# Kernel optimization log

Measured on AMD Instinct MI355X. Metric: run time of the kernel, lower is better.

## Reference

```python
import jax, jax.numpy as jnp
import numpy as np

EMBED_DIM = 1024
ATTEN_DIM = 64


def setup_inputs() -> dict:
    key = jax.random.key(0)
    k_x, k_q, k_k, k_v = jax.random.split(key, 4)
    B, S = 4, 4096
    scale = 1.0 / np.sqrt(EMBED_DIM)
    x = jax.random.normal(k_x, (B, S, EMBED_DIM), dtype=jnp.float32)
    # torch nn.Linear weights are [out_features, in_features]
    Wq = jax.random.normal(k_q, (ATTEN_DIM, EMBED_DIM), dtype=jnp.float32) * scale
    Wk = jax.random.normal(k_k, (ATTEN_DIM, EMBED_DIM), dtype=jnp.float32) * scale
    Wv = jax.random.normal(k_v, (ATTEN_DIM, EMBED_DIM), dtype=jnp.float32) * scale
    return {"x": x, "Wq": Wq, "Wk": Wk, "Wv": Wv}


def reference(x, Wq, Wk, Wv):
    # q, k, v: [B, S, D]
    q = jnp.einsum('bse,de->bsd', x, Wq)
    k = jnp.einsum('bse,de->bsd', x, Wk)
    v = jnp.einsum('bse,de->bsd', x, Wv)
    d = k.shape[-1]
    scores = jnp.einsum('bsd,btd->bst', q, k) / jnp.sqrt(jnp.float32(d))
    S = x.shape[1]
    causal = jnp.tril(jnp.ones((S, S), dtype=bool))
    scores = jnp.where(causal[None, :, :], scores, -jnp.inf)
    attn = jax.nn.softmax(scores, axis=-1)
    return jnp.einsum('bst,btd->bsd', attn, v)
```

## Files before the change

### kernel.cpp

```cpp
#include <hip/hip_runtime.h>
#include <hip/hip_bf16.h>
#include <stdint.h>

typedef __attribute__((ext_vector_type(8))) short  short8;
typedef __attribute__((ext_vector_type(4))) short  short4v;
typedef __attribute__((ext_vector_type(4))) float  float4v;

#define MFMA16(a, b, c) __builtin_amdgcn_mfma_f32_16x16x32_bf16((a), (b), (c), 0, 0, 0)

#define S_LEN  4096
#define NBATCH 4
#define EMB    1024
#define DD     64
#define NROWS  (NBATCH * S_LEN)
#define SCL2   0.1803368801111204f

#define AS1 const __attribute__((address_space(1))) unsigned int*
#define AS3 __attribute__((address_space(3))) unsigned int*

static __device__ __forceinline__ short f2bf(float f) {
  uint32_t u = __float_as_uint(f);
  return (short)((u + 0x7FFFu + ((u >> 16) & 1u)) >> 16);
}
static __device__ __forceinline__ unsigned pk2(float a, float b) {
  union { __hip_bfloat162 h; unsigned u; } z;
  z.h = __float22bfloat162_rn(make_float2(a, b));
  return z.u;
}
static __device__ __forceinline__ short8 cvt8(float4v a, float4v b) {
  union { unsigned u[4]; short8 s; } z;
  z.u[0] = pk2(a[0], a[1]); z.u[1] = pk2(a[2], a[3]);
  z.u[2] = pk2(b[0], b[1]); z.u[3] = pk2(b[2], b[3]);
  return z.s;
}

__global__ void wcvt_kernel(const float* __restrict__ Wq, const float* __restrict__ Wk,
                            const float* __restrict__ Wv, short* __restrict__ Wb2) {
  const int t   = blockIdx.x * 256 + threadIdx.x;
  const int row = t >> 7;
  const int k   = (t & 127) * 8;
  const float* src = (row < 64) ? (Wq + (size_t)row * EMB)
                   : (row < 128) ? (Wk + (size_t)(row - 64) * EMB)
                                 : (Wv + (size_t)(row - 128) * EMB);
  const float sc = (row < 64) ? SCL2 : 1.0f;
  float4v a = *(const float4v*)(src + k);
  float4v b = *(const float4v*)(src + k + 4);
#pragma unroll
  for (int i = 0; i < 4; ++i) { a[i] *= sc; b[i] *= sc; }
  *(short8*)(Wb2 + (((k >> 5) * 192 + row) << 5) + (k & 31)) = cvt8(a, b);
}

__global__ __launch_bounds__(256, 2) void qkv_kernel(
    const float* __restrict__ x, const short* __restrict__ Wb2,
    short* __restrict__ Qb, short* __restrict__ Kb, short* __restrict__ Vt) {
  __shared__ float As[2][2048];
  __shared__ short Bs[2][12288];

  const int tid  = threadIdx.x;
  const int w    = tid >> 6;
  const int lane = tid & 63;
  const int ln   = lane & 15;
  const int quad = lane >> 4;
  const int m0   = blockIdx.x * 32;
  const int wr   = w & 1;
  const int wc   = w >> 1;

  const int tA0 = 2 * w, tA1 = 2 * w + 1;
  const float* xA0 = x + (size_t)(m0 + ((tA0 >> 2) << 4) + (lane >> 2)) * EMB
                       + ((tA0 & 3) * 4 + (lane & 3)) * 4;
  const float* xA1 = x + (size_t)(m0 + ((tA1 >> 2) << 4) + (lane >> 2)) * EMB
                       + ((tA1 & 3) * 4 + (lane & 3)) * 4;
  const short* wB = Wb2 + (size_t)(6 * w) * 512 + lane * 8;

#define STAGE(S, BUF) do {                                                      \
    __builtin_amdgcn_global_load_lds((AS1)(xA0 + (S) * 64),                     \
        (AS3)&As[BUF][tA0 * 256], 16, 0, 0);                                    \
    __builtin_amdgcn_global_load_lds((AS1)(xA1 + (S) * 64),                     \
        (AS3)&As[BUF][tA1 * 256], 16, 0, 0);                                    \
    _Pragma("unroll")                                                           \
    for (int j = 0; j < 6; ++j)                                                 \
      __builtin_amdgcn_global_load_lds((AS1)(wB + (size_t)(S) * 12288 + j * 512),\
          (AS3)&Bs[BUF][(6 * w + j) * 512], 16, 0, 0);                          \
  } while (0)

  const float4v zz = {0.f, 0.f, 0.f, 0.f};
  float4v acc[6] = {zz, zz, zz, zz, zz, zz};

  STAGE(0, 0);
  int buf = 0;
  for (int s = 0; s < 16; ++s) {
    __syncthreads();
    if (s + 1 < 16) STAGE(s + 1, buf ^ 1);
    short8 aF[2];
#pragma unroll
    for (int h = 0; h < 2; ++h) {
      const int ai = (wr * 4 + 2 * h + (quad >> 1)) * 256 + (ln * 4 + (quad & 1) * 2) * 4;
      const float4v lo = *(const float4v*)&As[buf][ai];
      const float4v hi = *(const float4v*)&As[buf][ai + 4];
      aF[h] = cvt8(lo, hi);
    }
#pragma unroll
    for (int f = 0; f < 6; ++f) {
      const int cf = wc * 6 + f;
      const short8 b0 = *(const short8*)&Bs[buf][(cf * 16 + ln) * 32 + quad * 8];
      const short8 b1 = *(const short8*)&Bs[buf][6144 + (cf * 16 + ln) * 32 + quad * 8];
      if (wc == 0 || f < 2) {
        acc[f] = MFMA16(aF[0], b0, acc[f]);
        acc[f] = MFMA16(aF[1], b1, acc[f]);
      } else {
        acc[f] = MFMA16(b0, aF[0], acc[f]);
        acc[f] = MFMA16(b1, aF[1], acc[f]);
      }
    }
    buf ^= 1;
  }
#undef STAGE

  const int b  = m0 >> 12;
  const int sb = m0 & (S_LEN - 1);
  if (wc == 0) {
#pragma unroll
    for (int f = 0; f < 6; ++f)
#pragma unroll
      for (int r = 0; r < 4; ++r) {
        const int row = m0 + wr * 16 + quad * 4 + r;
        if (f < 4) Qb[(size_t)row * DD + f * 16 + ln] = f2bf(acc[f][r]);
        else       Kb[(size_t)row * DD + (f - 4) * 16 + ln] = f2bf(acc[f][r]);
      }
  } else {
#pragma unroll
    for (int f = 0; f < 2; ++f)
#pragma unroll
      for (int r = 0; r < 4; ++r) {
        const int row = m0 + wr * 16 + quad * 4 + r;
        Kb[(size_t)row * DD + 32 + f * 16 + ln] = f2bf(acc[f][r]);
      }
#pragma unroll
    for (int f = 2; f < 6; ++f)
#pragma unroll
      for (int r = 0; r < 4; ++r) {
        const int d = (f - 2) * 16 + quad * 4 + r;
        Vt[((size_t)b * DD + d) * S_LEN + sb + wr * 16 + ln] = f2bf(acc[f][r]);
      }
  }
}

__global__ __launch_bounds__(256, 2) void attn_kernel(
    const short* __restrict__ Qb, const short* __restrict__ Kb,
    const short* __restrict__ Vt, float* __restrict__ out) {
  __shared__ short kvbuf[4][2][4096];
  __shared__ float pbuf[4][16 * 36];
  __shared__ float llds[4][16];

  const int tid  = threadIdx.x;
  const int w    = tid >> 6;
  const int lane = tid & 63;
  const int ln   = lane & 15;
  const int quad = lane >> 4;
  const int g    = blockIdx.x;
  const int b    = g & 3;
  const int j    = g >> 2;

  const short* Kbase = Kb + (size_t)b * S_LEN * DD;
  const short* Vbase = Vt + (size_t)b * DD * S_LEN;
  const int koff = (lane & 7) * DD + (lane >> 3) * 8;
  const size_t voff = (size_t)(lane & 15) * S_LEN + (lane >> 4) * 8;
  float* pw = &pbuf[w][0];
  const float4v zz = {0.f, 0.f, 0.f, 0.f};

#define KVSTAGE(KV0, BUF) do {                                                  \
    const short* kp_ = Kbase + (size_t)(KV0) * DD + koff;                       \
    const short* vp_ = Vbase + (KV0) + voff;                                    \
    _Pragma("unroll")                                                           \
    for (int s5 = 0; s5 < 4; ++s5)                                              \
      __builtin_amdgcn_global_load_lds((AS1)(kp_ + s5 * 8 * DD),                \
          (AS3)&kvbuf[w][BUF][s5 * 512], 16, 0, 0);                             \
    _Pragma("unroll")                                                           \
    for (int s5 = 0; s5 < 4; ++s5)                                              \
      __builtin_amdgcn_global_load_lds((AS1)(vp_ + (size_t)(s5 * 16) * S_LEN),  \
          (AS3)&kvbuf[w][BUF][2048 + s5 * 512], 16, 0, 0);                      \
  } while (0)

  for (int ph = 0; ph < 2; ++ph) {
    const int band = ph ? (255 - j) : j;
    const int qb   = band * 16;
    const int qg0  = b * S_LEN + qb;
    const int T    = (qb + 47) >> 5;

    short8 aQ[2];
#pragma unroll
    for (int h = 0; h < 2; ++h)
      aQ[h] = *(const short8*)(Qb + (size_t)(qg0 + ln) * DD + h * 32 + quad * 8);

    float4v o[4] = {zz, zz, zz, zz};
    float lp[4]  = {0.f, 0.f, 0.f, 0.f};

    if (w < T) KVSTAGE(w * 32, 0);
    int buf = 0;

    for (int it = w; it < T; it += 4) {
      const int kv0 = it * 32;
      asm volatile("s_waitcnt vmcnt(0)" ::: "memory");
      const short* kb_ = &kvbuf[w][buf][0];
      const short* vb_ = &kvbuf[w][buf][2048];

      short8 kf[2][2];
#pragma unroll
      for (int ct = 0; ct < 2; ++ct)
#pragma unroll
        for (int h = 0; h < 2; ++h)
          kf[ct][h] = *(const short8*)(kb_ + (ct * 2 + (ln >> 3)) * 512
                                           + (ln & 7) * 8 + (h * 4 + quad) * 64);
      short8 vf[4];
#pragma unroll
      for (int dt = 0; dt < 4; ++dt)
        vf[dt] = *(const short8*)(vb_ + dt * 512 + ln * 8 + quad * 128);
      asm volatile("s_waitcnt lgkmcnt(0)" ::: "memory");

      if (it + 4 < T) KVSTAGE((it + 4) * 32, buf ^ 1);

      float4v s[2] = {zz, zz};
#pragma unroll
      for (int ct = 0; ct < 2; ++ct)
#pragma unroll
        for (int h = 0; h < 2; ++h)
          s[ct] = MFMA16(aQ[h], kf[ct][h], s[ct]);

      if (kv0 + 31 > qb) {
#pragma unroll
        for (int ct = 0; ct < 2; ++ct)
#pragma unroll
          for (int r = 0; r < 4; ++r) {
            float e = __builtin_amdgcn_exp2f(fminf(s[ct][r], 60.0f));
            if (kv0 + ct * 16 + ln > qb + quad * 4 + r) e = 0.f;
            s[ct][r] = e;
          }
      } else {
#pragma unroll
        for (int ct = 0; ct < 2; ++ct)
#pragma unroll
          for (int r = 0; r < 4; ++r)
            s[ct][r] = __builtin_amdgcn_exp2f(fminf(s[ct][r], 60.0f));
      }
#pragma unroll
      for (int r = 0; r < 4; ++r) lp[r] += s[0][r] + s[1][r];

#pragma unroll
      for (int ct = 0; ct < 2; ++ct)
#pragma unroll
        for (int r = 0; r < 4; ++r)
          pw[(quad * 4 + r) * 36 + ct * 16 + ln] = s[ct][r];
      asm volatile("s_waitcnt lgkmcnt(0)" ::: "memory");
      const float4v lo = *(const float4v*)&pw[ln * 36 + quad * 8];
      const float4v hi = *(const float4v*)&pw[ln * 36 + quad * 8 + 4];
      const short8 aP = cvt8(lo, hi);
#pragma unroll
      for (int dt = 0; dt < 4; ++dt)
        o[dt] = MFMA16(aP, vf[dt], o[dt]);

      buf ^= 1;
    }

#pragma unroll
    for (int r = 0; r < 4; ++r) {
      float lr = lp[r];
      lr += __shfl_xor(lr, 1);
      lr += __shfl_xor(lr, 2);
      lr += __shfl_xor(lr, 4);
      lr += __shfl_xor(lr, 8);
      if (ln == 0) llds[w][quad * 4 + r] = lr;
    }
    float* ow = (float*)&kvbuf[w][0][0];
#pragma unroll
    for (int dt = 0; dt < 4; ++dt)
#pragma unroll
      for (int r = 0; r < 4; ++r)
        ow[(quad * 4 + r) * 64 + dt * 16 + ln] = o[dt][r];
    __syncthreads();

#pragma unroll
    for (int jj = 0; jj < 4; ++jj) {
      const int idx = tid + jj * 256;
      const int row = idx >> 6, col = idx & 63;
      float sum = 0.f, lt = 0.f;
#pragma unroll
      for (int wi = 0; wi < 4; ++wi) {
        sum += ((const float*)&kvbuf[wi][0][0])[row * 64 + col];
        lt  += llds[wi][row];
      }
      out[(size_t)(qg0 + row) * DD + col] = sum * __builtin_amdgcn_rcpf(lt);
    }
    __syncthreads();
  }
#undef KVSTAGE
}

extern "C" void kernel_launch(void* const* d_in, const int* in_sizes, int n_in,
                              void* d_out, int out_size, void* d_ws, size_t ws_size,
                              hipStream_t stream) {
  const float* x  = (const float*)d_in[0];
  const float* Wq = (const float*)d_in[1];
  const float* Wk = (const float*)d_in[2];
  const float* Wv = (const float*)d_in[3];

  short* Qb  = (short*)d_ws;
  short* Kb  = Qb + (size_t)NROWS * DD;
  short* Vt  = Kb + (size_t)NROWS * DD;
  short* Wb2 = Vt + (size_t)NROWS * DD;

  wcvt_kernel<<<dim3(96), dim3(256), 0, stream>>>(Wq, Wk, Wv, Wb2);
  qkv_kernel<<<dim3(NROWS / 32), dim3(256), 0, stream>>>(x, Wb2, Qb, Kb, Vt);
  attn_kernel<<<dim3(NBATCH * 128), dim3(256), 0, stream>>>(Qb, Kb, Vt, (float*)d_out);
}
```

Measured before the change: 180.4 us.

## Process 32-row query bands with triple-buffered swizzled K/V staging

Each block now handles 32 query rows per band instead of 16, so every K/V tile loaded into LDS is reused by two MFMA row fragments. K/V staging becomes triple-buffered with a partial vmcnt wait, and LDS layouts use XOR swizzles to avoid bank conflicts. The grid halves to 256 blocks at one block per CU, trading occupancy for reuse and deeper prefetch.

```diff
diff --git a/kernel.cpp b/kernel.cpp
--- a/kernel.cpp
+++ b/kernel.cpp
@@ -145,12 +145,14 @@
   }
 }
 
-__global__ __launch_bounds__(256, 2) void attn_kernel(
+#define PSTRW 34
+
+__global__ __launch_bounds__(256, 1) void attn_kernel(
     const short* __restrict__ Qb, const short* __restrict__ Kb,
     const short* __restrict__ Vt, float* __restrict__ out) {
-  __shared__ short kvbuf[4][2][4096];
-  __shared__ float pbuf[4][16 * 36];
-  __shared__ float llds[4][16];
+  __shared__ short kvbuf[4][3][4096];
+  __shared__ float pbuf[4][32 * PSTRW];
+  __shared__ float llds[4][32];
 
   const int tid  = threadIdx.x;
   const int w    = tid >> 6;
@@ -163,14 +165,14 @@
 
   const short* Kbase = Kb + (size_t)b * S_LEN * DD;
   const short* Vbase = Vt + (size_t)b * DD * S_LEN;
-  const int koff = (lane & 7) * DD + (lane >> 3) * 8;
-  const size_t voff = (size_t)(lane & 15) * S_LEN + (lane >> 4) * 8;
+  const int    klane = (lane >> 3) * DD + (((lane & 7) ^ (lane >> 3))) * 8;
+  const size_t vlane = (size_t)(lane >> 2) * S_LEN + (((lane & 3) ^ ((lane >> 2) & 3))) * 8;
   float* pw = &pbuf[w][0];
   const float4v zz = {0.f, 0.f, 0.f, 0.f};
 
 #define KVSTAGE(KV0, BUF) do {                                                  \
-    const short* kp_ = Kbase + (size_t)(KV0) * DD + koff;                       \
-    const short* vp_ = Vbase + (KV0) + voff;                                    \
+    const short* kp_ = Kbase + (size_t)(KV0) * DD + klane;                      \
+    const short* vp_ = Vbase + (KV0) + vlane;                                   \
     _Pragma("unroll")                                                           \
     for (int s5 = 0; s5 < 4; ++s5)                                              \
       __builtin_amdgcn_global_load_lds((AS1)(kp_ + s5 * 8 * DD),                \
@@ -182,104 +184,133 @@
   } while (0)
 
   for (int ph = 0; ph < 2; ++ph) {
-    const int band = ph ? (255 - j) : j;
-    const int qb   = band * 16;
+    const int band = ph ? (127 - j) : j;
+    const int qb   = band * 32;
     const int qg0  = b * S_LEN + qb;
-    const int T    = (qb + 47) >> 5;
-
-    short8 aQ[2];
-#pragma unroll
-    for (int h = 0; h < 2; ++h)
-      aQ[h] = *(const short8*)(Qb + (size_t)(qg0 + ln) * DD + h * 32 + quad * 8);
-
-    float4v o[4] = {zz, zz, zz, zz};
-    float lp[4]  = {0.f, 0.f, 0.f, 0.f};
-
-    if (w < T) KVSTAGE(w * 32, 0);
-    int buf = 0;
+    const int T    = band + 1;
+
+    short8 aQ[2][2];
+#pragma unroll
+    for (int rfi = 0; rfi < 2; ++rfi)
+#pragma unroll
+      for (int h = 0; h < 2; ++h)
+        aQ[rfi][h] = *(const short8*)(Qb + (size_t)(qg0 + rfi * 16 + ln) * DD + h * 32 + quad * 8);
+
+    float4v o[2][4];
+    float lp[2][4];
+#pragma unroll
+    for (int rfi = 0; rfi < 2; ++rfi)
+#pragma unroll
+      for (int d = 0; d < 4; ++d) { o[rfi][d] = zz; lp[rfi][d] = 0.f; }
+
+    if (w < T)     KVSTAGE(w * 32, 0);
+    if (w + 4 < T) KVSTAGE((w + 4) * 32, 1);
+    int nbuf = 0;
 
     for (int it = w; it < T; it += 4) {
       const int kv0 = it * 32;
-      asm volatile("s_waitcnt vmcnt(0)" ::: "memory");
-      const short* kb_ = &kvbuf[w][buf][0];
-      const short* vb_ = &kvbuf[w][buf][2048];
+      if (it + 4 < T) { asm volatile("s_waitcnt vmcnt(8)" ::: "memory"); }
+      else            { asm volatile("s_waitcnt vmcnt(0)" ::: "memory"); }
+      const short* kb_ = &kvbuf[w][nbuf][0];
+      const short* vb_ = &kvbuf[w][nbuf][2048];
 
       short8 kf[2][2];
 #pragma unroll
       for (int ct = 0; ct < 2; ++ct)
 #pragma unroll
         for (int h = 0; h < 2; ++h)
-          kf[ct][h] = *(const short8*)(kb_ + (ct * 2 + (ln >> 3)) * 512
-                                           + (ln & 7) * 8 + (h * 4 + quad) * 64);
+          kf[ct][h] = *(const short8*)(kb_ + (2 * ct + (ln >> 3)) * 512
+                                           + (ln & 7) * 64 + (((h * 4 + quad) ^ (ln & 7))) * 8);
       short8 vf[4];
 #pragma unroll
       for (int dt = 0; dt < 4; ++dt)
-        vf[dt] = *(const short8*)(vb_ + dt * 512 + ln * 8 + quad * 128);
+        vf[dt] = *(const short8*)(vb_ + dt * 512 + ln * 32 + ((quad ^ (ln & 3))) * 8);
       asm volatile("s_waitcnt lgkmcnt(0)" ::: "memory");
 
-      if (it + 4 < T) KVSTAGE((it + 4) * 32, buf ^ 1);
-
-      float4v s[2] = {zz, zz};
-#pragma unroll
-      for (int ct = 0; ct < 2; ++ct)
-#pragma unroll
-        for (int h = 0; h < 2; ++h)
-          s[ct] = MFMA16(aQ[h], kf[ct][h], s[ct]);
-
-      if (kv0 + 31 > qb) {
+      if (it + 8 < T) KVSTAGE((it + 8) * 32, (nbuf + 2 >= 3) ? (nbuf - 1) : (nbuf + 2));
+
+      float4v s[2][2];
+#pragma unroll
+      for (int rfi = 0; rfi < 2; ++rfi)
+#pragma unroll
+        for (int ct = 0; ct < 2; ++ct) {
+          s[rfi][ct] = MFMA16(aQ[rfi][0], kf[ct][0], zz);
+          s[rfi][ct] = MFMA16(aQ[rfi][1], kf[ct][1], s[rfi][ct]);
+        }
+
+      if (it == band) {
+#pragma unroll
+        for (int rfi = 0; rfi < 2; ++rfi)
+#pragma unroll
+          for (int ct = 0; ct < 2; ++ct)
+#pragma unroll
+            for (int r = 0; r < 4; ++r) {
+              float e = __builtin_amdgcn_exp2f(fminf(s[rfi][ct][r], 60.0f));
+              if (kv0 + ct * 16 + ln > qb + rfi * 16 + quad * 4 + r) e = 0.f;
+              s[rfi][ct][r] = e;
+            }
+      } else {
+#pragma unroll
+        for (int rfi = 0; rfi < 2; ++rfi)
+#pragma unroll
+          for (int ct = 0; ct < 2; ++ct)
+#pragma unroll
+            for (int r = 0; r < 4; ++r)
+              s[rfi][ct][r] = __builtin_amdgcn_exp2f(fminf(s[rfi][ct][r], 60.0f));
+      }
+#pragma unroll
+      for (int rfi = 0; rfi < 2; ++rfi)
+#pragma unroll
+        for (int r = 0; r < 4; ++r)
+          lp[rfi][r] += s[rfi][0][r] + s[rfi][1][r];
+
+#pragma unroll
+      for (int rfi = 0; rfi < 2; ++rfi)
 #pragma unroll
         for (int ct = 0; ct < 2; ++ct)
 #pragma unroll
-          for (int r = 0; r < 4; ++r) {
-            float e = __builtin_amdgcn_exp2f(fminf(s[ct][r], 60.0f));
-            if (kv0 + ct * 16 + ln > qb + quad * 4 + r) e = 0.f;
-            s[ct][r] = e;
-          }
-      } else {
-#pragma unroll
-        for (int ct = 0; ct < 2; ++ct)
-#pragma unroll
           for (int r = 0; r < 4; ++r)
-            s[ct][r] = __builtin_amdgcn_exp2f(fminf(s[ct][r], 60.0f));
-      }
-#pragma unroll
-      for (int r = 0; r < 4; ++r) lp[r] += s[0][r] + s[1][r];
-
-#pragma unroll
-      for (int ct = 0; ct < 2; ++ct)
+            pw[(rfi * 16 + quad * 4 + r) * PSTRW + ct * 16 + ln] = s[rfi][ct][r];
+      asm volatile("s_waitcnt lgkmcnt(0)" ::: "memory");
+      short8 aP[2];
+#pragma unroll
+      for (int rfi = 0; rfi < 2; ++rfi) {
+        const float4v lo = *(const float4v*)&pw[(rfi * 16 + ln) * PSTRW + quad * 8];
+        const float4v hi = *(const float4v*)&pw[(rfi * 16 + ln) * PSTRW + quad * 8 + 4];
+        aP[rfi] = cvt8(lo, hi);
+      }
+#pragma unroll
+      for (int rfi = 0; rfi < 2; ++rfi)
+#pragma unroll
+        for (int dt = 0; dt < 4; ++dt)
+          o[rfi][dt] = MFMA16(aP[rfi], vf[dt], o[rfi][dt]);
+
+      nbuf = (nbuf + 1 >= 3) ? 0 : nbuf + 1;
+    }
+
+#pragma unroll
+    for (int rfi = 0; rfi < 2; ++rfi)
+#pragma unroll
+      for (int r = 0; r < 4; ++r) {
+        float lr = lp[rfi][r];
+        lr += __shfl_xor(lr, 1);
+        lr += __shfl_xor(lr, 2);
+        lr += __shfl_xor(lr, 4);
+        lr += __shfl_xor(lr, 8);
+        if (ln == 0) llds[w][rfi * 16 + quad * 4 + r] = lr;
+      }
+    float* ow = (float*)&kvbuf[w][0][0];
+#pragma unroll
+    for (int rfi = 0; rfi < 2; ++rfi)
+#pragma unroll
+      for (int dt = 0; dt < 4; ++dt)
 #pragma unroll
         for (int r = 0; r < 4; ++r)
-          pw[(quad * 4 + r) * 36 + ct * 16 + ln] = s[ct][r];
-      asm volatile("s_waitcnt lgkmcnt(0)" ::: "memory");
-      const float4v lo = *(const float4v*)&pw[ln * 36 + quad * 8];
-      const float4v hi = *(const float4v*)&pw[ln * 36 + quad * 8 + 4];
-      const short8 aP = cvt8(lo, hi);
-#pragma unroll
-      for (int dt = 0; dt < 4; ++dt)
-        o[dt] = MFMA16(aP, vf[dt], o[dt]);
-
-      buf ^= 1;
-    }
-
-#pragma unroll
-    for (int r = 0; r < 4; ++r) {
-      float lr = lp[r];
-      lr += __shfl_xor(lr, 1);
-      lr += __shfl_xor(lr, 2);
-      lr += __shfl_xor(lr, 4);
-      lr += __shfl_xor(lr, 8);
-      if (ln == 0) llds[w][quad * 4 + r] = lr;
-    }
-    float* ow = (float*)&kvbuf[w][0][0];
-#pragma unroll
-    for (int dt = 0; dt < 4; ++dt)
-#pragma unroll
-      for (int r = 0; r < 4; ++r)
-        ow[(quad * 4 + r) * 64 + dt * 16 + ln] = o[dt][r];
+          ow[(rfi * 16 + quad * 4 + r) * 64 + dt * 16 + ln] = o[rfi][dt][r];
     __syncthreads();
 
 #pragma unroll
-    for (int jj = 0; jj < 4; ++jj) {
+    for (int jj = 0; jj < 8; ++jj) {
       const int idx = tid + jj * 256;
       const int row = idx >> 6, col = idx & 63;
       float sum = 0.f, lt = 0.f;
@@ -310,5 +341,5 @@
 
   wcvt_kernel<<<dim3(96), dim3(256), 0, stream>>>(Wq, Wk, Wv, Wb2);
   qkv_kernel<<<dim3(NROWS / 32), dim3(256), 0, stream>>>(x, Wb2, Qb, Kb, Vt);
-  attn_kernel<<<dim3(NBATCH * 128), dim3(256), 0, stream>>>(Qb, Kb, Vt, (float*)d_out);
-}
+  attn_kernel<<<dim3(NBATCH * 64), dim3(256), 0, stream>>>(Qb, Kb, Vt, (float*)d_out);
+}
```

Measured after the change: 162.1 us. 10.1% less time.

## Share swizzled K/V tiles across 8 waves with 32-row query bands

Applied to the files above, without the earlier changes.

The attention kernel moves from 256-thread blocks, where each wave streamed its own private K/V slices, to 512-thread blocks. Eight waves (2 query halves × 4 key quarters) now share a block-wide double-buffered 128-key K/V tile in LDS, and each block handles 32 query rows per band. The LDS layouts are XOR-swizzled to avoid bank conflicts, and the causal mask is applied only on the last tile. This cuts redundant global K/V traffic per query row, at the cost of a block barrier every iteration, half as many blocks (256), and a wider cross-wave reduction at the end.

```diff
diff --git a/kernel.cpp b/kernel.cpp
--- a/kernel.cpp
+++ b/kernel.cpp
@@ -145,94 +145,97 @@
   }
 }
 
-__global__ __launch_bounds__(256, 2) void attn_kernel(
+__global__ __launch_bounds__(512, 1) void attn_kernel(
     const short* __restrict__ Qb, const short* __restrict__ Kb,
     const short* __restrict__ Vt, float* __restrict__ out) {
-  __shared__ short kvbuf[4][2][4096];
-  __shared__ float pbuf[4][16 * 36];
-  __shared__ float llds[4][16];
+  __shared__ short Ks[2][8192];
+  __shared__ short Vs[2][8192];
+  __shared__ float pbuf[8][16 * 34];
+  __shared__ float llds[8][16];
 
   const int tid  = threadIdx.x;
   const int w    = tid >> 6;
   const int lane = tid & 63;
   const int ln   = lane & 15;
   const int quad = lane >> 4;
+  const int qh   = w & 1;
+  const int kh   = w >> 1;
   const int g    = blockIdx.x;
   const int b    = g & 3;
   const int j    = g >> 2;
 
   const short* Kbase = Kb + (size_t)b * S_LEN * DD;
   const short* Vbase = Vt + (size_t)b * DD * S_LEN;
-  const int koff = (lane & 7) * DD + (lane >> 3) * 8;
-  const size_t voff = (size_t)(lane & 15) * S_LEN + (lane >> 4) * 8;
   float* pw = &pbuf[w][0];
   const float4v zz = {0.f, 0.f, 0.f, 0.f};
 
+  const int kT0 = 2 * w, kT1 = 2 * w + 1;
+  const int kR0 = 8 * kT0 + (lane >> 3), kR1 = 8 * kT1 + (lane >> 3);
+  const int kC  = ((lane & 7) ^ (lane >> 3)) * 8;
+  const int vU0 = 2 * w, vU1 = 2 * w + 1;
+  const int vR0 = 4 * vU0 + (lane >> 4), vR1 = 4 * vU1 + (lane >> 4);
+  const int vC0 = (((lane & 15) ^ (lane >> 4)) & 15) * 8;
+  const int vC1 = ((((lane & 15) ^ (lane >> 4)) ^ 4) & 15) * 8;
+
 #define KVSTAGE(KV0, BUF) do {                                                  \
-    const short* kp_ = Kbase + (size_t)(KV0) * DD + koff;                       \
-    const short* vp_ = Vbase + (KV0) + voff;                                    \
-    _Pragma("unroll")                                                           \
-    for (int s5 = 0; s5 < 4; ++s5)                                              \
-      __builtin_amdgcn_global_load_lds((AS1)(kp_ + s5 * 8 * DD),                \
-          (AS3)&kvbuf[w][BUF][s5 * 512], 16, 0, 0);                             \
-    _Pragma("unroll")                                                           \
-    for (int s5 = 0; s5 < 4; ++s5)                                              \
-      __builtin_amdgcn_global_load_lds((AS1)(vp_ + (size_t)(s5 * 16) * S_LEN),  \
-          (AS3)&kvbuf[w][BUF][2048 + s5 * 512], 16, 0, 0);                      \
+    __builtin_amdgcn_global_load_lds((AS1)(Kbase + (size_t)((KV0) + kR0) * DD + kC), \
+        (AS3)&Ks[BUF][kT0 * 512], 16, 0, 0);                                    \
+    __builtin_amdgcn_global_load_lds((AS1)(Kbase + (size_t)((KV0) + kR1) * DD + kC), \
+        (AS3)&Ks[BUF][kT1 * 512], 16, 0, 0);                                    \
+    __builtin_amdgcn_global_load_lds((AS1)(Vbase + (KV0) + (size_t)vR0 * S_LEN + vC0), \
+        (AS3)&Vs[BUF][vU0 * 512], 16, 0, 0);                                    \
+    __builtin_amdgcn_global_load_lds((AS1)(Vbase + (KV0) + (size_t)vR1 * S_LEN + vC1), \
+        (AS3)&Vs[BUF][vU1 * 512], 16, 0, 0);                                    \
   } while (0)
 
   for (int ph = 0; ph < 2; ++ph) {
-    const int band = ph ? (255 - j) : j;
-    const int qb   = band * 16;
+    const int band = ph ? (127 - j) : j;
+    const int qb   = band * 32;
     const int qg0  = b * S_LEN + qb;
-    const int T    = (qb + 47) >> 5;
+    const int T    = (qb + 159) >> 7;
 
     short8 aQ[2];
 #pragma unroll
     for (int h = 0; h < 2; ++h)
-      aQ[h] = *(const short8*)(Qb + (size_t)(qg0 + ln) * DD + h * 32 + quad * 8);
+      aQ[h] = *(const short8*)(Qb + (size_t)(qg0 + qh * 16 + ln) * DD + h * 32 + quad * 8);
 
     float4v o[4] = {zz, zz, zz, zz};
     float lp[4]  = {0.f, 0.f, 0.f, 0.f};
 
-    if (w < T) KVSTAGE(w * 32, 0);
-    int buf = 0;
-
-    for (int it = w; it < T; it += 4) {
-      const int kv0 = it * 32;
-      asm volatile("s_waitcnt vmcnt(0)" ::: "memory");
-      const short* kb_ = &kvbuf[w][buf][0];
-      const short* vb_ = &kvbuf[w][buf][2048];
+    KVSTAGE(0, 0);
+    for (int it = 0; it < T; ++it) {
+      __syncthreads();
+      if (it + 1 < T) KVSTAGE((it + 1) * 128, (it + 1) & 1);
+      const int buf = it & 1;
+      const int kv0 = it * 128;
 
       short8 kf[2][2];
 #pragma unroll
       for (int ct = 0; ct < 2; ++ct)
 #pragma unroll
         for (int h = 0; h < 2; ++h)
-          kf[ct][h] = *(const short8*)(kb_ + (ct * 2 + (ln >> 3)) * 512
-                                           + (ln & 7) * 8 + (h * 4 + quad) * 64);
+          kf[ct][h] = *(const short8*)&Ks[buf][(kh * 4 + ct * 2 + (ln >> 3)) * 512
+                          + (ln & 7) * 64 + (((h * 4 + quad) ^ (ln & 7))) * 8];
       short8 vf[4];
 #pragma unroll
       for (int dt = 0; dt < 4; ++dt)
-        vf[dt] = *(const short8*)(vb_ + dt * 512 + ln * 8 + quad * 128);
-      asm volatile("s_waitcnt lgkmcnt(0)" ::: "memory");
-
-      if (it + 4 < T) KVSTAGE((it + 4) * 32, buf ^ 1);
-
-      float4v s[2] = {zz, zz};
-#pragma unroll
-      for (int ct = 0; ct < 2; ++ct)
-#pragma unroll
-        for (int h = 0; h < 2; ++h)
-          s[ct] = MFMA16(aQ[h], kf[ct][h], s[ct]);
-
-      if (kv0 + 31 > qb) {
+        vf[dt] = *(const short8*)&Vs[buf][(dt * 4 + (ln >> 2)) * 512 + (ln & 3) * 128
+                          + ((((kh * 4 + quad) ^ (ln & 3) ^ (((ln >> 2) & 1) * 4)) & 15)) * 8];
+
+      float4v s[2];
+#pragma unroll
+      for (int ct = 0; ct < 2; ++ct) {
+        s[ct] = MFMA16(aQ[0], kf[ct][0], zz);
+        s[ct] = MFMA16(aQ[1], kf[ct][1], s[ct]);
+      }
+
+      if (it == T - 1) {
 #pragma unroll
         for (int ct = 0; ct < 2; ++ct)
 #pragma unroll
           for (int r = 0; r < 4; ++r) {
             float e = __builtin_amdgcn_exp2f(fminf(s[ct][r], 60.0f));
-            if (kv0 + ct * 16 + ln > qb + quad * 4 + r) e = 0.f;
+            if (kv0 + kh * 32 + ct * 16 + ln > qb + qh * 16 + quad * 4 + r) e = 0.f;
             s[ct][r] = e;
           }
       } else {
@@ -249,17 +252,16 @@
       for (int ct = 0; ct < 2; ++ct)
 #pragma unroll
         for (int r = 0; r < 4; ++r)
-          pw[(quad * 4 + r) * 36 + ct * 16 + ln] = s[ct][r];
+          pw[(quad * 4 + r) * 34 + ct * 16 + ln] = s[ct][r];
       asm volatile("s_waitcnt lgkmcnt(0)" ::: "memory");
-      const float4v lo = *(const float4v*)&pw[ln * 36 + quad * 8];
-      const float4v hi = *(const float4v*)&pw[ln * 36 + quad * 8 + 4];
+      const float4v lo = *(const float4v*)&pw[ln * 34 + quad * 8];
+      const float4v hi = *(const float4v*)&pw[ln * 34 + quad * 8 + 4];
       const short8 aP = cvt8(lo, hi);
 #pragma unroll
       for (int dt = 0; dt < 4; ++dt)
         o[dt] = MFMA16(aP, vf[dt], o[dt]);
-
-      buf ^= 1;
-    }
+    }
+    __syncthreads();
 
 #pragma unroll
     for (int r = 0; r < 4; ++r) {
@@ -270,23 +272,23 @@
       lr += __shfl_xor(lr, 8);
       if (ln == 0) llds[w][quad * 4 + r] = lr;
     }
-    float* ow = (float*)&kvbuf[w][0][0];
+    float* ow = (float*)&Ks[0][0];
 #pragma unroll
     for (int dt = 0; dt < 4; ++dt)
 #pragma unroll
       for (int r = 0; r < 4; ++r)
-        ow[(quad * 4 + r) * 64 + dt * 16 + ln] = o[dt][r];
+        ow[kh * 2048 + (qh * 16 + quad * 4 + r) * 64 + dt * 16 + ln] = o[dt][r];
     __syncthreads();
 
 #pragma unroll
     for (int jj = 0; jj < 4; ++jj) {
-      const int idx = tid + jj * 256;
+      const int idx = tid + jj * 512;
       const int row = idx >> 6, col = idx & 63;
       float sum = 0.f, lt = 0.f;
 #pragma unroll
-      for (int wi = 0; wi < 4; ++wi) {
-        sum += ((const float*)&kvbuf[wi][0][0])[row * 64 + col];
-        lt  += llds[wi][row];
+      for (int k4 = 0; k4 < 4; ++k4) {
+        sum += ow[k4 * 2048 + idx];
+        lt  += llds[(row >> 4) + 2 * k4][row & 15];
       }
       out[(size_t)(qg0 + row) * DD + col] = sum * __builtin_amdgcn_rcpf(lt);
     }
@@ -310,5 +312,5 @@
 
   wcvt_kernel<<<dim3(96), dim3(256), 0, stream>>>(Wq, Wk, Wv, Wb2);
   qkv_kernel<<<dim3(NROWS / 32), dim3(256), 0, stream>>>(x, Wb2, Qb, Kb, Vt);
-  attn_kernel<<<dim3(NBATCH * 128), dim3(256), 0, stream>>>(Qb, Kb, Vt, (float*)d_out);
-}
+  attn_kernel<<<dim3(NBATCH * 64), dim3(512), 0, stream>>>(Qb, Kb, Vt, (float*)d_out);
+}
```

New measurement: 165.4 us. -8.3%, faster.
